# Kernel tuning notes

Measured on AMD Instinct MI355X. Metric: run time of the kernel, lower is better.

Reference implementation:

```python
import jax, jax.numpy as jnp
import numpy as np

DIM, H, C = 1024, 16, 64
D = DIM // H  # head_dim = 64
GATE_HID = 16


def setup_inputs() -> dict:
    key = jax.random.key(0)
    ks = jax.random.split(key, 8)
    B, L = 2, 2048

    def xav(k, fan_in, fan_out):
        return jax.random.normal(k, (fan_in, fan_out), jnp.float32) * np.sqrt(2.0 / (fan_in + fan_out))

    return {
        "x": jax.random.normal(ks[0], (B, L, DIM), jnp.float32),
        "Wq": xav(ks[1], DIM, DIM), "bq": jnp.zeros((DIM,), jnp.float32),
        "Wk": xav(ks[2], DIM, DIM), "bk": jnp.zeros((DIM,), jnp.float32),
        "Wv": xav(ks[3], DIM, DIM), "bv": jnp.zeros((DIM,), jnp.float32),
        "Wg1": xav(ks[4], DIM, GATE_HID), "bg1": jnp.zeros((GATE_HID,), jnp.float32),
        "Wg2": xav(ks[5], GATE_HID, H * D), "bg2": jnp.zeros((H * D,), jnp.float32),
    }


def reference(x, Wq, bq, Wk, bk, Wv, bv, Wg1, bg1, Wg2, bg2):
    B, L, dim = x.shape
    pad = (-L) % C
    if pad:
        x = jnp.pad(x, ((0, 0), (0, pad), (0, 0)))
    Lp = L + pad

    def proj(W, b):
        # (B, Lp, dim) -> (B, H, Lp, D)
        return (x @ W + b).reshape(B, Lp, H, D).transpose(0, 2, 1, 3)

    q, k, v = proj(Wq, bq), proj(Wk, bk), proj(Wv, bv)
    gate = jax.nn.sigmoid(jax.nn.silu(x @ Wg1 + bg1) @ Wg2 + bg2)
    alpha = 0.9 * gate.reshape(B, Lp, H, D).transpose(0, 2, 1, 3) + 0.1  # (B,H,Lp,D)

    # --- intra-chunk causal softmax attention (vectorized over chunks) ---
    Nc = Lp // C
    qc = q.reshape(B, H, Nc, C, D)
    kc = k.reshape(B, H, Nc, C, D)
    vc = v.reshape(B, H, Nc, C, D)
    scores = jnp.einsum('bhncd,bhnkd->bhnck', qc, kc) / np.sqrt(D).astype(np.float32)
    causal = jnp.tril(jnp.ones((C, C), bool))
    scores = jnp.where(causal, scores, -jnp.inf)
    intra = jnp.einsum('bhnck,bhnke->bhnce', jax.nn.softmax(scores, axis=-1), vc)
    intra = intra.reshape(B, H, Lp, D)

    # --- inter: gated linear-attention recurrence over the full sequence ---
    # Note: in the original code S is updated every timestep (including inside
    # chunks), so the 'inter' term at step t sees ALL tokens < t, not just
    # previous chunks.
    def step(S, inp):
        q_t, k_t, v_t, a_t = inp  # each (B, H, D)
        inter_t = jnp.einsum('bhd,bhde->bhe', q_t, S)
        S = a_t[..., None] * S + k_t[..., None] * v_t[..., None, :]
        return S, inter_t

    xs = tuple(a.transpose(2, 0, 1, 3) for a in (q, k, v, alpha))  # (Lp, B, H, D)
    S0 = jnp.zeros((B, H, D, D), x.dtype)
    _, inter = jax.lax.scan(step, S0, xs)  # (Lp, B, H, D)
    inter = inter.transpose(1, 2, 0, 3)  # (B, H, Lp, D)

    out = (inter + intra).transpose(0, 2, 1, 3).reshape(B, Lp, dim)
    return out[:, :L]
```

## Files before the change

### kernel.cpp

```cpp
#include <hip/hip_runtime.h>
#include <math.h>

#define DIMN 1024
#define NH 16
#define HD 64
#define CHK 64
#define NB 2
#define SEQ 2048
#define NTOK (NB*SEQ)
#define NCHUNK (SEQ/CHK)
#define GH 16

typedef __bf16 bf16x8 __attribute__((ext_vector_type(8)));
typedef float f32x4 __attribute__((ext_vector_type(4)));
typedef unsigned short u16x4 __attribute__((ext_vector_type(4)));

__device__ __forceinline__ unsigned short f2bf(float f) {
  union { float f; unsigned u; } a; a.f = f;
  unsigned r = a.u + 0x7FFFu + ((a.u >> 16) & 1u);
  return (unsigned short)(r >> 16);
}
__device__ __forceinline__ float bf2f(unsigned short v) {
  union { unsigned u; float f; } a; a.u = ((unsigned)v) << 16;
  return a.f;
}

__device__ __forceinline__ void gload16(const void* g, void* l) {
  __builtin_amdgcn_global_load_lds(
      (const __attribute__((address_space(1))) void*)g,
      (__attribute__((address_space(3))) void*)l, 16, 0, 0);
}

__global__ __launch_bounds__(256) void k_cast_wT(const float* __restrict__ W0,
    const float* __restrict__ W1, const float* __restrict__ W2,
    unsigned short* __restrict__ wt) {
  __shared__ float tile[64][68];
  int z = blockIdx.z;
  const float* W = z==0 ? W0 : z==1 ? W1 : W2;
  unsigned short* o = wt + (size_t)z*DIMN*DIMN;
  int k0 = blockIdx.y*64, n0 = blockIdx.x*64;
  int tr = threadIdx.x >> 4, c0 = (threadIdx.x & 15)*4;
  #pragma unroll
  for (int s = 0; s < 4; ++s) {
    int r = tr + s*16;
    *(f32x4*)&tile[r][c0] = *(const f32x4*)(W + (size_t)(k0+r)*DIMN + n0 + c0);
  }
  __syncthreads();
  #pragma unroll
  for (int s = 0; s < 4; ++s) {
    int nn = tr + s*16;
    ushort4 v;
    v.x = f2bf(tile[c0+0][nn]);
    v.y = f2bf(tile[c0+1][nn]);
    v.z = f2bf(tile[c0+2][nn]);
    v.w = f2bf(tile[c0+3][nn]);
    *(ushort4*)(o + (size_t)(n0+nn)*DIMN + k0 + c0) = v;
  }
}

__global__ __launch_bounds__(256) void k_wg1t(const float* __restrict__ Wg1,
    unsigned short* __restrict__ wg1b) {
  int idx = blockIdx.x*256 + threadIdx.x;
  int k = idx & 1023, j = idx >> 10;
  wg1b[j*DIMN + k] = f2bf(Wg1[k*GH + j]);
}

__global__ __launch_bounds__(256) void k_castx_hidden(const float* __restrict__ x,
    const unsigned short* __restrict__ wg1b, const float* __restrict__ bg1,
    unsigned short* __restrict__ xb, float* __restrict__ hid) {
  __shared__ __align__(16) unsigned short xs[16][1032];
  __shared__ float red[4][16][16];
  int tid = threadIdx.x;
  size_t base = (size_t)blockIdx.x * 16 * DIMN;
  #pragma unroll
  for (int i = 0; i < 16; ++i) {
    int idx4 = tid + i*256;
    int r = idx4 >> 8, c4 = idx4 & 255;
    f32x4 v = *(const f32x4*)(x + base + (size_t)idx4*4);
    u16x4 o;
    o[0]=f2bf(v[0]); o[1]=f2bf(v[1]); o[2]=f2bf(v[2]); o[3]=f2bf(v[3]);
    *(u16x4*)&xs[r][c4*4] = o;
    *(u16x4*)(xb + base + (size_t)idx4*4) = o;
  }
  __syncthreads();
  int l = tid & 63, w = tid >> 6;
  int lr = l & 15, kg = l >> 4;
  union FB { uint4 u; bf16x8 h; } a, b;
  f32x4 acc = {0.f,0.f,0.f,0.f};
  const unsigned short* wrow = wg1b + (size_t)lr*DIMN + w*256 + kg*8;
  #pragma unroll
  for (int kk = 0; kk < 8; ++kk) {
    a.u = *(const uint4*)&xs[lr][w*256 + kk*32 + kg*8];
    b.u = *(const uint4*)(wrow + kk*32);
    acc = __builtin_amdgcn_mfma_f32_16x16x32_bf16(a.h, b.h, acc, 0, 0, 0);
  }
  #pragma unroll
  for (int rg = 0; rg < 4; ++rg) red[w][kg*4 + rg][lr] = acc[rg];
  __syncthreads();
  {
    int m = tid >> 4, j = tid & 15;
    float s = red[0][m][j] + red[1][m][j] + red[2][m][j] + red[3][m][j];
    s += bg1[j];
    hid[(blockIdx.x*16 + m)*GH + j] = s / (1.f + expf(-s));
  }
}

__global__ __launch_bounds__(256, 3) void k_projqkv(const unsigned short* __restrict__ xb,
    const unsigned short* __restrict__ wt,
    const float* __restrict__ b0, const float* __restrict__ b1, const float* __restrict__ b2,
    unsigned short* __restrict__ o0, unsigned short* __restrict__ o1,
    unsigned short* __restrict__ o2) {
  __shared__ unsigned short As[3][128*32];
  __shared__ unsigned short Bs[3][128*32];
  int tid = threadIdx.x;
  int wg = blockIdx.y * gridDim.x + blockIdx.x;
  int swz = (wg & 7) * 96 + (wg >> 3);
  int bx = swz % 24, by = swz / 24;
  int n3 = bx*128;
  int z = n3 >> 10;
  int n0l = n3 & 1023;
  const float* bias = z==0 ? b0 : z==1 ? b1 : b2;
  unsigned short* out = z==0 ? o0 : z==1 ? o1 : o2;
  int m0 = by*128;

  int l = tid & 63;
  int w = tid >> 6;
  int wr = w >> 1, wc = w & 1;
  int lrow = l & 15, kg = l >> 4;

  f32x4 acc[4][4] = {};

  int r0s = tid >> 2, s0s = tid & 3;
  int r1s = (tid + 256) >> 2;
  int sg0 = s0s ^ ((r0s >> 1) & 3);
  int sg1 = s0s ^ ((r1s >> 1) & 3);

  #define STAGE(buf, kt) do { \
    int kb_ = (kt)*32; \
    gload16(xb + ((size_t)(m0 + r0s)*DIMN + kb_ + sg0*8), &As[buf][tid*8]); \
    gload16(wt + ((size_t)(n3 + r0s)*DIMN + kb_ + sg0*8), &Bs[buf][tid*8]); \
    gload16(xb + ((size_t)(m0 + r1s)*DIMN + kb_ + sg1*8), &As[buf][(tid+256)*8]); \
    gload16(wt + ((size_t)(n3 + r1s)*DIMN + kb_ + sg1*8), &Bs[buf][(tid+256)*8]); \
  } while (0)

  STAGE(0, 0);
  STAGE(1, 1);
  for (int t = 0; t < DIMN/32; ++t) {
    if (t < DIMN/32 - 1) {
      asm volatile("s_waitcnt vmcnt(4)" ::: "memory");
    } else {
      asm volatile("s_waitcnt vmcnt(0)" ::: "memory");
    }
    __builtin_amdgcn_s_barrier();
    if (t+2 < DIMN/32) STAGE((t+2)%3, t+2);
    int buf = t % 3;
    union { uint4 u; bf16x8 h; } af[4], bfr[4];
    #pragma unroll
    for (int mf = 0; mf < 4; ++mf) {
      int r = wr*64 + mf*16 + lrow;
      int slot = kg ^ ((r >> 1) & 3);
      af[mf].u = *(const uint4*)&As[buf][r*32 + slot*8];
    }
    #pragma unroll
    for (int nf = 0; nf < 4; ++nf) {
      int r = wc*64 + nf*16 + lrow;
      int slot = kg ^ ((r >> 1) & 3);
      bfr[nf].u = *(const uint4*)&Bs[buf][r*32 + slot*8];
    }
    #pragma unroll
    for (int mf = 0; mf < 4; ++mf)
      #pragma unroll
      for (int nf = 0; nf < 4; ++nf)
        acc[mf][nf] = __builtin_amdgcn_mfma_f32_16x16x32_bf16(
            af[mf].h, bfr[nf].h, acc[mf][nf], 0, 0, 0);
  }
  #undef STAGE

  float bv[4];
  #pragma unroll
  for (int nf = 0; nf < 4; ++nf) bv[nf] = bias[n0l + wc*64 + nf*16 + lrow];
  #pragma unroll
  for (int mf = 0; mf < 4; ++mf) {
    int rbase = m0 + wr*64 + mf*16 + kg*4;
    #pragma unroll
    for (int nf = 0; nf < 4; ++nf) {
      int c = n0l + wc*64 + nf*16 + lrow;
      #pragma unroll
      for (int rg = 0; rg < 4; ++rg)
        out[(size_t)(rbase+rg)*DIMN + c] = f2bf(acc[mf][nf][rg] + bv[nf]);
    }
  }
}

__global__ __launch_bounds__(256, 4) void k_ginc(const unsigned short* __restrict__ kbuf,
    const unsigned short* __restrict__ vbuf,
    const float* __restrict__ hid, const float* __restrict__ Wg2,
    const float* __restrict__ bg2,
    unsigned short* __restrict__ G, float* __restrict__ Bv) {
  __shared__ __align__(16) unsigned short kb16[64*72];
  __shared__ __align__(16) unsigned short vT[64*72];
  __shared__ __align__(16) unsigned short kdT[64*72];
  __shared__ __align__(16) float scr[2048];
  __shared__ float seg[4][64];
  int tid = threadIdx.x;
  int bid = blockIdx.x;
  int bh = bid >> 5, n = bid & 31;
  int b = bh >> 4, h = bh & 15;
  int colbase = h*HD;
  size_t rowbase = (size_t)b*SEQ + n*CHK;

  {
    int r = tid >> 2, j0 = (tid & 3)*4;
    *(f32x4*)&scr[r*16 + j0] = *(const f32x4*)(hid + (rowbase + r)*GH + j0);
    int j = tid >> 4, d0 = (tid & 15)*4;
    *(f32x4*)&scr[1024 + j*64 + d0] = *(const f32x4*)(Wg2 + (size_t)j*DIMN + colbase + d0);
  }
  #pragma unroll
  for (int i = 0; i < 4; ++i) {
    int f4 = tid + i*256;
    int r = f4 >> 4, cg = f4 & 15, c0 = cg*4;
    size_t g = (rowbase + r)*DIMN + colbase + c0;
    u16x4 k4 = *(const u16x4*)(kbuf + g);
    u16x4 v4 = *(const u16x4*)(vbuf + g);
    *(u16x4*)&kb16[r*72 + c0] = k4;
    #pragma unroll
    for (int j = 0; j < 4; ++j) vT[(c0+j)*72 + r] = v4[j];
  }
  __syncthreads();

  {
    int d = tid & 63, ig = tid >> 6;
    float wcol[16];
    #pragma unroll
    for (int j = 0; j < 16; ++j) wcol[j] = scr[1024 + j*64 + d];
    float bgd = bg2[colbase + d];
    float P[16];
    float run = 0.f;
    #pragma unroll
    for (int t = 0; t < 16; ++t) {
      int i = ig*16 + t;
      float acc = bgd;
      #pragma unroll
      for (int j = 0; j < 16; ++j) acc = fmaf(scr[i*16 + j], wcol[j], acc);
      float gg = 1.f/(1.f + expf(-acc));
      run += log2f(fmaf(0.9f, gg, 0.1f));
      P[t] = run;
    }
    seg[ig][d] = run;
    __syncthreads();
    float s0 = seg[0][d], s1 = seg[1][d], s2 = seg[2][d], s3 = seg[3][d];
    float carry = (ig > 0 ? s0 : 0.f) + (ig > 1 ? s1 : 0.f) + (ig > 2 ? s2 : 0.f);
    float Lb63 = s0 + s1 + s2 + s3;
    if (ig == 0) Bv[(size_t)bid*HD + d] = exp2f(Lb63);
    union { unsigned short s[16]; uint4 u[2]; } kd;
    #pragma unroll
    for (int t = 0; t < 16; ++t) {
      int i = ig*16 + t;
      float kv = bf2f(kb16[i*72 + d]);
      kd.s[t] = f2bf(kv * exp2f(Lb63 - carry - P[t]));
    }
    *(uint4*)&kdT[d*72 + ig*16] = kd.u[0];
    *(uint4*)&kdT[d*72 + ig*16 + 8] = kd.u[1];
  }
  __syncthreads();

  int l = tid & 63, w = tid >> 6;
  int lr = l & 15, kg = l >> 4;
  int ks = kg*8;
  int arow = w*16 + lr;
  union FB { uint4 u; bf16x8 h; } a0, a1;
  a0.u = *(const uint4*)&kdT[arow*72 + ks];
  a1.u = *(const uint4*)&kdT[arow*72 + 32 + ks];
  unsigned short* gp = G + (size_t)bid*(HD*HD);
  #pragma unroll
  for (int nf = 0; nf < 4; ++nf) {
    FB b0v, b1v;
    b0v.u = *(const uint4*)&vT[(nf*16+lr)*72 + ks];
    b1v.u = *(const uint4*)&vT[(nf*16+lr)*72 + 32 + ks];
    f32x4 z = {0.f,0.f,0.f,0.f};
    z = __builtin_amdgcn_mfma_f32_16x16x32_bf16(a0.h, b0v.h, z, 0,0,0);
    z = __builtin_amdgcn_mfma_f32_16x16x32_bf16(a1.h, b1v.h, z, 0,0,0);
    #pragma unroll
    for (int rg = 0; rg < 4; ++rg)
      gp[(w*16 + kg*4 + rg)*HD + nf*16 + lr] = f2bf(z[rg]);
  }
}

__global__ __launch_bounds__(256) void k_scan(unsigned short* __restrict__ buf,
    const float* __restrict__ Bv) {
  int idx = blockIdx.x*256 + threadIdx.x;
  int e = idx & 63, d = (idx >> 6) & 63, bh = idx >> 12;
  unsigned short* gp = buf + (size_t)bh*NCHUNK*HD*HD + d*HD + e;
  const float* bp = Bv + (size_t)bh*NCHUNK*HD + d;
  float g[NCHUNK], bb[NCHUNK];
  #pragma unroll
  for (int n = 0; n < NCHUNK; ++n) g[n] = bf2f(gp[n*(HD*HD)]);
  #pragma unroll
  for (int n = 0; n < NCHUNK; ++n) bb[n] = bp[n*HD];
  float s = 0.f;
  #pragma unroll
  for (int n = 0; n < NCHUNK; ++n) {
    gp[n*(HD*HD)] = f2bf(s);
    s = fmaf(bb[n], s, g[n]);
  }
}

__global__ __launch_bounds__(256) void k_chunk(const unsigned short* __restrict__ qbuf,
    const unsigned short* __restrict__ kbuf, const unsigned short* __restrict__ vbuf,
    const float* __restrict__ hid, const float* __restrict__ Wg2,
    const float* __restrict__ bg2,
    const unsigned short* __restrict__ states, float* __restrict__ outp) {
  __shared__ __align__(16) unsigned short qb16[64*72];
  __shared__ __align__(16) unsigned short kb16[64*72];
  __shared__ __align__(16) unsigned short vT[64*72];
  __shared__ __align__(16) unsigned short Pl[64*72];
  __shared__ __align__(16) unsigned short Swt[2][64*72];
  __shared__ __align__(16) float lb[65*68];
  __shared__ __align__(16) unsigned short dgs[4][16*40];
  __shared__ float seg[4][64];

  const int tid = threadIdx.x;
  const int bid = blockIdx.x;
  const int bh = bid >> 5, n = bid & 31;
  const int b = bh >> 4, h = bh & 15;
  const int colbase = h*HD;
  const size_t rowbase = (size_t)b*SEQ + n*CHK;
  const unsigned short* stp = states + (size_t)(bh*NCHUNK + n)*(HD*HD);

  float* scr = (float*)Pl;
  {
    int r = tid >> 2, j0 = (tid & 3)*4;
    *(f32x4*)&scr[r*16 + j0] = *(const f32x4*)(hid + (rowbase + r)*GH + j0);
    int j = tid >> 4, d0 = (tid & 15)*4;
    *(f32x4*)&scr[1024 + j*64 + d0] = *(const f32x4*)(Wg2 + (size_t)j*DIMN + colbase + d0);
  }
  #pragma unroll
  for (int i = 0; i < 4; ++i) {
    int f4 = tid + i*256;
    int r = f4 >> 4, cg = f4 & 15, c0 = cg*4;
    size_t g = (rowbase + r)*DIMN + colbase + c0;
    u16x4 q4 = *(const u16x4*)(qbuf + g);
    u16x4 k4 = *(const u16x4*)(kbuf + g);
    u16x4 v4 = *(const u16x4*)(vbuf + g);
    u16x4 s4 = *(const u16x4*)(stp + r*HD + c0);
    #pragma unroll
    for (int j = 0; j < 4; ++j) {
      vT[(c0+j)*72 + r] = v4[j];
      Swt[0][(c0+j)*72 + r] = s4[j];
    }
    *(u16x4*)&qb16[r*72 + c0] = q4;
    *(u16x4*)&kb16[r*72 + c0] = k4;
  }
  __syncthreads();

  {
    int r = tid >> 2, db = (tid & 3)*16;
    float av[16];
    #pragma unroll
    for (int dq = 0; dq < 16; ++dq) {
      int d = db + dq;
      float acc = bg2[colbase + d];
      #pragma unroll
      for (int j = 0; j < GH; ++j)
        acc = fmaf(scr[r*16 + j], scr[1024 + j*64 + d], acc);
      float gg = 1.f/(1.f + expf(-acc));
      av[dq] = log2f(fmaf(0.9f, gg, 0.1f));
    }
    #pragma unroll
    for (int dq = 0; dq < 16; dq += 4) {
      f32x4 v4 = {av[dq], av[dq+1], av[dq+2], av[dq+3]};
      *(f32x4*)&lb[r*68 + db + dq] = v4;
    }
  }
  __syncthreads();

  {
    int d = tid & 63, ww = tid >> 6;
    float run = 0.f;
    #pragma unroll
    for (int ii = 0; ii < 16; ++ii) {
      int i = ww*16 + ii;
      float t = lb[i*68 + d];
      lb[i*68 + d] = run;
      run += t;
    }
    seg[ww][d] = run;
  }
  __syncthreads();
  {
    int d = tid & 63, ww = tid >> 6;
    float carry = 0.f;
    for (int w2 = 0; w2 < ww; ++w2) carry += seg[w2][d];
    if (ww > 0)
      for (int ii = 0; ii < 16; ++ii) lb[(ww*16+ii)*68 + d] += carry;
    if (ww == 3) lb[64*68 + d] = carry + seg[3][d];
  }
  __syncthreads();

  const int l = tid & 63, w = tid >> 6;
  const int lr = l & 15, lg = l >> 4;
  const int ks = lg*8;
  const int arow = w*16 + lr;

  union FB { uint4 u; bf16x8 h; unsigned short s[8]; };

  FB qa0, qa1;
  qa0.u = *(const uint4*)&qb16[arow*72 + ks];
  qa1.u = *(const uint4*)&qb16[arow*72 + 32 + ks];
  f32x4 sc[4];
  #pragma unroll
  for (int nf = 0; nf < 4; ++nf) {
    FB b0, b1;
    b0.u = *(const uint4*)&kb16[(nf*16+lr)*72 + ks];
    b1.u = *(const uint4*)&kb16[(nf*16+lr)*72 + 32 + ks];
    f32x4 z = {0.f,0.f,0.f,0.f};
    z = __builtin_amdgcn_mfma_f32_16x16x32_bf16(qa0.h, b0.h, z, 0,0,0);
    z = __builtin_amdgcn_mfma_f32_16x16x32_bf16(qa1.h, b1.h, z, 0,0,0);
    sc[nf] = z;
  }

  float rmax[4] = {-3e38f,-3e38f,-3e38f,-3e38f};
  #pragma unroll
  for (int nf = 0; nf < 4; ++nf) {
    int col = nf*16 + lr;
    #pragma unroll
    for (int rg = 0; rg < 4; ++rg) {
      int row = w*16 + lg*4 + rg;
      float v = sc[nf][rg]*0.125f;
      if (col > row) v = -1e30f;
      sc[nf][rg] = v;
      rmax[rg] = fmaxf(rmax[rg], v);
    }
  }
  #pragma unroll
  for (int m = 1; m <= 8; m <<= 1)
    #pragma unroll
    for (int rg = 0; rg < 4; ++rg)
      rmax[rg] = fmaxf(rmax[rg], __shfl_xor(rmax[rg], m));
  float rsum[4] = {0.f,0.f,0.f,0.f};
  #pragma unroll
  for (int nf = 0; nf < 4; ++nf)
    #pragma unroll
    for (int rg = 0; rg < 4; ++rg) {
      float e = exp2f((sc[nf][rg] - rmax[rg])*1.44269504f);
      sc[nf][rg] = e;
      rsum[rg] += e;
    }
  #pragma unroll
  for (int m = 1; m <= 8; m <<= 1)
    #pragma unroll
    for (int rg = 0; rg < 4; ++rg)
      rsum[rg] += __shfl_xor(rsum[rg], m);
  __syncthreads();
  #pragma unroll
  for (int nf = 0; nf < 4; ++nf)
    #pragma unroll
    for (int rg = 0; rg < 4; ++rg)
      Pl[(w*16 + lg*4 + rg)*72 + nf*16 + lr] = f2bf(sc[nf][rg]);
  float inv[4];
  #pragma unroll
  for (int rg = 0; rg < 4; ++rg) inv[rg] = 1.f/rsum[rg];
  __syncthreads();

  f32x4 acc[4];
  {
    FB p0, p1;
    p0.u = *(const uint4*)&Pl[arow*72 + ks];
    p1.u = *(const uint4*)&Pl[arow*72 + 32 + ks];
    #pragma unroll
    for (int nf = 0; nf < 4; ++nf) {
      FB v0, v1;
      v0.u = *(const uint4*)&vT[(nf*16+lr)*72 + ks];
      v1.u = *(const uint4*)&vT[(nf*16+lr)*72 + 32 + ks];
      f32x4 z = {0.f,0.f,0.f,0.f};
      z = __builtin_amdgcn_mfma_f32_16x16x32_bf16(p0.h, v0.h, z, 0,0,0);
      z = __builtin_amdgcn_mfma_f32_16x16x32_bf16(p1.h, v1.h, z, 0,0,0);
      #pragma unroll
      for (int rg = 0; rg < 4; ++rg)
        acc[nf][rg] = z[rg]*inv[rg];
    }
  }

  {
    int dA = arow;
    float lb32 = lb[32*68 + dA];
    FB ku;
    #pragma unroll
    for (int j = 0; j < 8; ++j) {
      int s = ks + j;
      float kv = bf2f(kb16[s*72 + dA]);
      ku.s[j] = f2bf(kv * exp2f(lb32 - lb[(s+1)*68 + dA]));
    }
    int d0 = w*16 + lg*4;
    float bs[4];
    #pragma unroll
    for (int rg = 0; rg < 4; ++rg) bs[rg] = exp2f(lb[32*68 + d0 + rg]);
    #pragma unroll
    for (int nf = 0; nf < 4; ++nf) {
      int e = nf*16 + lr;
      FB vv;
      vv.u = *(const uint4*)&vT[e*72 + ks];
      f32x4 z = {0.f,0.f,0.f,0.f};
      z = __builtin_amdgcn_mfma_f32_16x16x32_bf16(ku.h, vv.h, z, 0,0,0);
      u16x4 s0v = *(const u16x4*)&Swt[0][e*72 + d0];
      u16x4 s1v;
      #pragma unroll
      for (int rg = 0; rg < 4; ++rg)
        s1v[rg] = f2bf(z[rg] + bs[rg]*bf2f(s0v[rg]));
      *(u16x4*)&Swt[1][e*72 + d0] = s1v;
    }
  }
  __syncthreads();

  {
    const int T = (w >= 2) ? 32 : 0;
    const unsigned short* Ssel = (w >= 2) ? &Swt[1][0] : &Swt[0][0];
    FB qd[2];
    #pragma unroll
    for (int kst = 0; kst < 2; ++kst) {
      int ds = kst*32 + ks;
      f32x4 lbi0 = *(const f32x4*)&lb[arow*68 + ds];
      f32x4 lbi1 = *(const f32x4*)&lb[arow*68 + ds + 4];
      f32x4 lbt0 = *(const f32x4*)&lb[T*68 + ds];
      f32x4 lbt1 = *(const f32x4*)&lb[T*68 + ds + 4];
      FB qr;
      qr.u = *(const uint4*)&qb16[arow*72 + ds];
      #pragma unroll
      for (int j = 0; j < 4; ++j) {
        qd[kst].s[j]   = f2bf(bf2f(qr.s[j])   * exp2f(lbi0[j] - lbt0[j]));
        qd[kst].s[4+j] = f2bf(bf2f(qr.s[4+j]) * exp2f(lbi1[j] - lbt1[j]));
      }
    }
    #pragma unroll
    for (int nf = 0; nf < 4; ++nf) {
      FB s0f, s1f;
      s0f.u = *(const uint4*)&Ssel[(nf*16+lr)*72 + ks];
      s1f.u = *(const uint4*)&Ssel[(nf*16+lr)*72 + 32 + ks];
      acc[nf] = __builtin_amdgcn_mfma_f32_16x16x32_bf16(qd[0].h, s0f.h, acc[nf], 0,0,0);
      acc[nf] = __builtin_amdgcn_mfma_f32_16x16x32_bf16(qd[1].h, s1f.h, acc[nf], 0,0,0);
    }
    const int nb_ = (w & 1) ? 2 : 1;
    f32x4 dgc[2] = {{0.f,0.f,0.f,0.f},{0.f,0.f,0.f,0.f}};
    #pragma unroll
    for (int bf_ = 0; bf_ < 2; ++bf_) {
      if (bf_ < nb_) {
        int s = T + bf_*16 + lr;
        f32x4 z = {0.f,0.f,0.f,0.f};
        #pragma unroll
        for (int kst = 0; kst < 2; ++kst) {
          int ds = kst*32 + ks;
          f32x4 lbt0 = *(const f32x4*)&lb[T*68 + ds];
          f32x4 lbt1 = *(const f32x4*)&lb[T*68 + ds + 4];
          f32x4 lbs0 = *(const f32x4*)&lb[(s+1)*68 + ds];
          f32x4 lbs1 = *(const f32x4*)&lb[(s+1)*68 + ds + 4];
          FB kr, kd;
          kr.u = *(const uint4*)&kb16[s*72 + ds];
          #pragma unroll
          for (int j = 0; j < 4; ++j) {
            kd.s[j]   = f2bf(bf2f(kr.s[j])   * exp2f(lbt0[j] - lbs0[j]));
            kd.s[4+j] = f2bf(bf2f(kr.s[4+j]) * exp2f(lbt1[j] - lbs1[j]));
          }
          z = __builtin_amdgcn_mfma_f32_16x16x32_bf16(qd[kst].h, kd.h, z, 0,0,0);
        }
        dgc[bf_] = z;
      }
    }
    int iis = (w & 1)*16 + lg*4;
    #pragma unroll
    for (int bf_ = 0; bf_ < 2; ++bf_) {
      #pragma unroll
      for (int rg = 0; rg < 4; ++rg) {
        int ssu = bf_*16 + lr;
        float v = (bf_ < nb_ && ssu < iis + rg) ? dgc[bf_][rg] : 0.f;
        dgs[w][(lg*4 + rg)*40 + bf_*16 + lr] = f2bf(v);
      }
    }
    FB dga;
    dga.u = *(const uint4*)&dgs[w][lr*40 + ks];
    #pragma unroll
    for (int nf = 0; nf < 4; ++nf) {
      FB vv;
      vv.u = *(const uint4*)&vT[(nf*16+lr)*72 + T + ks];
      acc[nf] = __builtin_amdgcn_mfma_f32_16x16x32_bf16(dga.h, vv.h, acc[nf], 0,0,0);
    }
  }

  #pragma unroll
  for (int nf = 0; nf < 4; ++nf)
    #pragma unroll
    for (int rg = 0; rg < 4; ++rg)
      outp[(rowbase + w*16 + lg*4 + rg)*DIMN + colbase + nf*16 + lr] = acc[nf][rg];
}

extern "C" void kernel_launch(void* const* d_in, const int* in_sizes, int n_in,
                              void* d_out, int out_size, void* d_ws, size_t ws_size,
                              hipStream_t stream) {
  const float* x   = (const float*)d_in[0];
  const float* Wq  = (const float*)d_in[1];
  const float* bq  = (const float*)d_in[2];
  const float* Wk  = (const float*)d_in[3];
  const float* bk  = (const float*)d_in[4];
  const float* Wv  = (const float*)d_in[5];
  const float* bv  = (const float*)d_in[6];
  const float* Wg1 = (const float*)d_in[7];
  const float* bg1 = (const float*)d_in[8];
  const float* Wg2 = (const float*)d_in[9];
  const float* bg2 = (const float*)d_in[10];
  float* out = (float*)d_out;

  float* ws = (float*)d_ws;
  const size_t NT = (size_t)NTOK*DIMN;
  const size_t NST = (size_t)NB*NH*NCHUNK*HD*HD;
  float* hid = ws;
  float* Bv  = hid + (size_t)NTOK*GH;
  unsigned short* stb = (unsigned short*)(Bv + (size_t)NB*NH*NCHUNK*HD);
  unsigned short* xb = stb + NST;
  unsigned short* wt = xb + NT;
  unsigned short* wg1b = wt + 3*(size_t)DIMN*DIMN;
  unsigned short* qb = wg1b + (size_t)GH*DIMN;
  unsigned short* kb = qb + NT;
  unsigned short* vb = kb + NT;

  k_cast_wT<<<dim3(16, 16, 3), 256, 0, stream>>>(Wq, Wk, Wv, wt);
  k_wg1t<<<(GH*DIMN)/256, 256, 0, stream>>>(Wg1, wg1b);
  k_castx_hidden<<<NTOK/16, 256, 0, stream>>>(x, wg1b, bg1, xb, hid);
  k_projqkv<<<dim3(24, 32), 256, 0, stream>>>(
      xb, wt, bq, bk, bv, qb, kb, vb);
  k_ginc<<<NB*NH*NCHUNK, 256, 0, stream>>>(kb, vb, hid, Wg2, bg2, stb, Bv);
  k_scan<<<(NB*NH*HD*HD)/256, 256, 0, stream>>>(stb, Bv);
  k_chunk<<<NB*NH*NCHUNK, 256, 0, stream>>>(qb, kb, vb, hid, Wg2, bg2, stb, out);
}
```

Measured before the change: 94.30 us.

## Fuse gate log-decay computation with prefix scan, drop barriers, add MFMA priority hints

```diff
diff --git a/kernel.cpp b/kernel.cpp
--- a/kernel.cpp
+++ b/kernel.cpp
@@ -331,8 +331,6 @@
   {
     int r = tid >> 2, j0 = (tid & 3)*4;
     *(f32x4*)&scr[r*16 + j0] = *(const f32x4*)(hid + (rowbase + r)*GH + j0);
-    int j = tid >> 4, d0 = (tid & 15)*4;
-    *(f32x4*)&scr[1024 + j*64 + d0] = *(const f32x4*)(Wg2 + (size_t)j*DIMN + colbase + d0);
   }
   #pragma unroll
   for (int i = 0; i < 4; ++i) {
@@ -354,46 +352,31 @@
   __syncthreads();
 
   {
-    int r = tid >> 2, db = (tid & 3)*16;
-    float av[16];
-    #pragma unroll
-    for (int dq = 0; dq < 16; ++dq) {
-      int d = db + dq;
-      float acc = bg2[colbase + d];
-      #pragma unroll
-      for (int j = 0; j < GH; ++j)
-        acc = fmaf(scr[r*16 + j], scr[1024 + j*64 + d], acc);
+    int d = tid & 63, ig = tid >> 6;
+    float wcol[16];
+    #pragma unroll
+    for (int j = 0; j < 16; ++j) wcol[j] = Wg2[(size_t)j*DIMN + colbase + d];
+    float bgd = bg2[colbase + d];
+    float Pex[16];
+    float run = 0.f;
+    #pragma unroll
+    for (int t = 0; t < 16; ++t) {
+      int i = ig*16 + t;
+      float acc = bgd;
+      #pragma unroll
+      for (int j = 0; j < 16; ++j) acc = fmaf(scr[i*16 + j], wcol[j], acc);
       float gg = 1.f/(1.f + expf(-acc));
-      av[dq] = log2f(fmaf(0.9f, gg, 0.1f));
-    }
-    #pragma unroll
-    for (int dq = 0; dq < 16; dq += 4) {
-      f32x4 v4 = {av[dq], av[dq+1], av[dq+2], av[dq+3]};
-      *(f32x4*)&lb[r*68 + db + dq] = v4;
-    }
-  }
-  __syncthreads();
-
-  {
-    int d = tid & 63, ww = tid >> 6;
-    float run = 0.f;
-    #pragma unroll
-    for (int ii = 0; ii < 16; ++ii) {
-      int i = ww*16 + ii;
-      float t = lb[i*68 + d];
-      lb[i*68 + d] = run;
-      run += t;
-    }
-    seg[ww][d] = run;
-  }
-  __syncthreads();
-  {
-    int d = tid & 63, ww = tid >> 6;
+      Pex[t] = run;
+      run += log2f(fmaf(0.9f, gg, 0.1f));
+    }
+    seg[ig][d] = run;
+    __syncthreads();
     float carry = 0.f;
-    for (int w2 = 0; w2 < ww; ++w2) carry += seg[w2][d];
-    if (ww > 0)
-      for (int ii = 0; ii < 16; ++ii) lb[(ww*16+ii)*68 + d] += carry;
-    if (ww == 3) lb[64*68 + d] = carry + seg[3][d];
+    for (int w2 = 0; w2 < ig; ++w2) carry += seg[w2][d];
+    #pragma unroll
+    for (int t = 0; t < 16; ++t)
+      lb[(ig*16 + t)*68 + d] = carry + Pex[t];
+    if (ig == 3) lb[64*68 + d] = carry + run;
   }
   __syncthreads();
 
@@ -408,6 +391,7 @@
   qa0.u = *(const uint4*)&qb16[arow*72 + ks];
   qa1.u = *(const uint4*)&qb16[arow*72 + 32 + ks];
   f32x4 sc[4];
+  __builtin_amdgcn_s_setprio(1);
   #pragma unroll
   for (int nf = 0; nf < 4; ++nf) {
     FB b0, b1;
@@ -418,6 +402,7 @@
     z = __builtin_amdgcn_mfma_f32_16x16x32_bf16(qa1.h, b1.h, z, 0,0,0);
     sc[nf] = z;
   }
+  __builtin_amdgcn_s_setprio(0);
 
   float rmax[4] = {-3e38f,-3e38f,-3e38f,-3e38f};
   #pragma unroll
@@ -451,7 +436,6 @@
     #pragma unroll
     for (int rg = 0; rg < 4; ++rg)
       rsum[rg] += __shfl_xor(rsum[rg], m);
-  __syncthreads();
   #pragma unroll
   for (int nf = 0; nf < 4; ++nf)
     #pragma unroll
@@ -467,6 +451,7 @@
     FB p0, p1;
     p0.u = *(const uint4*)&Pl[arow*72 + ks];
     p1.u = *(const uint4*)&Pl[arow*72 + 32 + ks];
+    __builtin_amdgcn_s_setprio(1);
     #pragma unroll
     for (int nf = 0; nf < 4; ++nf) {
       FB v0, v1;
@@ -479,6 +464,7 @@
       for (int rg = 0; rg < 4; ++rg)
         acc[nf][rg] = z[rg]*inv[rg];
     }
+    __builtin_amdgcn_s_setprio(0);
   }
 
   {
@@ -495,6 +481,7 @@
     float bs[4];
     #pragma unroll
     for (int rg = 0; rg < 4; ++rg) bs[rg] = exp2f(lb[32*68 + d0 + rg]);
+    __builtin_amdgcn_s_setprio(1);
     #pragma unroll
     for (int nf = 0; nf < 4; ++nf) {
       int e = nf*16 + lr;
@@ -509,6 +496,7 @@
         s1v[rg] = f2bf(z[rg] + bs[rg]*bf2f(s0v[rg]));
       *(u16x4*)&Swt[1][e*72 + d0] = s1v;
     }
+    __builtin_amdgcn_s_setprio(0);
   }
   __syncthreads();
 
@@ -531,6 +519,7 @@
         qd[kst].s[4+j] = f2bf(bf2f(qr.s[4+j]) * exp2f(lbi1[j] - lbt1[j]));
       }
     }
+    __builtin_amdgcn_s_setprio(1);
     #pragma unroll
     for (int nf = 0; nf < 4; ++nf) {
       FB s0f, s1f;
@@ -539,6 +528,7 @@
       acc[nf] = __builtin_amdgcn_mfma_f32_16x16x32_bf16(qd[0].h, s0f.h, acc[nf], 0,0,0);
       acc[nf] = __builtin_amdgcn_mfma_f32_16x16x32_bf16(qd[1].h, s1f.h, acc[nf], 0,0,0);
     }
+    __builtin_amdgcn_s_setprio(0);
     const int nb_ = (w & 1) ? 2 : 1;
     f32x4 dgc[2] = {{0.f,0.f,0.f,0.f},{0.f,0.f,0.f,0.f}};
     #pragma unroll
@@ -577,12 +567,14 @@
     }
     FB dga;
     dga.u = *(const uint4*)&dgs[w][lr*40 + ks];
+    __builtin_amdgcn_s_setprio(1);
     #pragma unroll
     for (int nf = 0; nf < 4; ++nf) {
       FB vv;
       vv.u = *(const uint4*)&vT[(nf*16+lr)*72 + T + ks];
       acc[nf] = __builtin_amdgcn_mfma_f32_16x16x32_bf16(dga.h, vv.h, acc[nf], 0,0,0);
     }
+    __builtin_amdgcn_s_setprio(0);
   }
 
   #pragma unroll
```

New measurement: 93.32 us, median of 2. About the same (-1.0%).
